# Kernel tuning notes

Hardware: AMD Instinct MI355X
Metric: run time of the kernel (lower is better)

## Reference

```python
import jax, jax.numpy as jnp
import numpy as np

NUM_LAYERS = 2
VOCAB = 32000
IN_FEAT = 256          # embedding dim is IN_FEAT-1, +1 for cue scalar
HIDDEN = 256
ATN = 64               # hardcoded atn_feature_size in GraphConvolution
CLASSES = 2
B, N = 8, 2048


def setup_inputs() -> dict:
    key = jax.random.key(0)
    ks = jax.random.split(key, 12)
    x = jax.random.randint(ks[0], (B, N), 0, VOCAB, dtype=jnp.int32)
    cue = jax.random.randint(ks[1], (B, N), 0, 2, dtype=jnp.int32)
    adj = (jax.random.uniform(ks[2], (B, N, N)) < 0.01).astype(jnp.float32)
    s = 1.0 / np.sqrt(HIDDEN)
    emb_table = jax.random.normal(ks[3], (VOCAB, IN_FEAT - 1), jnp.float32) * 0.02
    Wh = jax.random.uniform(ks[4], (IN_FEAT, HIDDEN), jnp.float32, -s, s)
    bh = jax.random.uniform(ks[5], (HIDDEN,), jnp.float32, -s, s)
    Wq = jax.random.uniform(ks[6], (HIDDEN, ATN), jnp.float32, -s, s)
    Wk = jax.random.uniform(ks[7], (HIDDEN, ATN), jnp.float32, -s, s)
    Wv = jax.random.uniform(ks[8], (HIDDEN, HIDDEN), jnp.float32, -s, s)
    gcb = jax.random.uniform(ks[9], (HIDDEN,), jnp.float32, -s, s)
    Wc = jax.random.uniform(ks[10], (HIDDEN, CLASSES), jnp.float32, -s, s)
    bc = jax.random.uniform(ks[11], (CLASSES,), jnp.float32, -s, s)
    return {"x": x, "cue": cue, "adj": adj, "emb_table": emb_table,
            "Wh": Wh, "bh": bh, "Wq": Wq, "Wk": Wk, "Wv": Wv,
            "gcb": gcb, "Wc": Wc, "bc": bc}


def graph_attention_layer(h, adj, Wq, Wk, Wv, gcb):
    # h: [B,N,H]; adj: [B,N,N] binary. Per node i: softmax over neighbors j of
    # (Wk h_j) . (Wq h_i), weighted sum of Wv h_j. Zero-degree nodes get 0 (pre-bias).
    q = jnp.einsum('bnh,ha->bna', h, Wq)        # [B,N,A]
    k = jnp.einsum('bnh,ha->bna', h, Wk)        # [B,N,A]
    v = jnp.einsum('bnh,hg->bng', h, Wv)        # [B,N,H]
    logits = jnp.einsum('bia,bja->bij', q, k)   # [B,N,N]
    mask = adj > 0
    attn = jax.nn.softmax(jnp.where(mask, logits, -1e9), axis=-1)
    out = jnp.einsum('bij,bjh->bih', attn, v)   # [B,N,H]
    has_nbr = jnp.any(mask, axis=-1, keepdims=True)  # [B,N,1]
    return jnp.where(has_nbr, out, 0.0) + gcb


def reference(x, cue, adj, emb_table, Wh, bh, Wq, Wk, Wv, gcb, Wc, bc):
    emb = emb_table[x]                                   # [B,N,IN_FEAT-1]
    feats = jnp.concatenate([emb, cue.astype(jnp.float32)[..., None]], axis=-1)
    h = jax.nn.relu(jnp.einsum('bnf,fh->bnh', feats, Wh) + bh)
    for _ in range(NUM_LAYERS):
        h = jax.nn.sigmoid(graph_attention_layer(h, adj, Wq, Wk, Wv, gcb))
    logits = jnp.einsum('bnh,hc->bnc', h, Wc) + bc
    return jax.nn.softmax(logits, axis=-1)
```

## Files before the change

### kernel.cpp

```cpp
#include <hip/hip_runtime.h>
#include <hip/hip_bf16.h>


#define NB 8
#define NN 2048
#define ROWS (NB * NN)
#define MAXD 64

typedef float f4 __attribute__((ext_vector_type(4)));
typedef short bf8 __attribute__((ext_vector_type(8)));
typedef unsigned short u16;
typedef u16 us4 __attribute__((ext_vector_type(4)));
typedef u16 us8 __attribute__((ext_vector_type(8)));

__device__ __forceinline__ float sigmoidf_(float x) { return 1.f / (1.f + __expf(-x)); }
__device__ __forceinline__ u16 f2bf(float f) {
    unsigned u = __float_as_uint(f);
    u += 0x7fffu + ((u >> 16) & 1u);
    return (u16)(u >> 16);
}
__device__ __forceinline__ float bf2f(u16 h) {
    return __uint_as_float(((unsigned)h) << 16);
}

#define PACK_BLKS 96
#define EMB_BLKS 512

__global__ __launch_bounds__(256) void k_fused_front(
        const int* __restrict__ x, const int* __restrict__ cue,
        const float* __restrict__ adj, const float* __restrict__ emb,
        const float* __restrict__ Wh, const float* __restrict__ bh,
        const float* __restrict__ Wq, const float* __restrict__ Wk,
        const float* __restrict__ Wv,
        u16* __restrict__ hB, u16* __restrict__ Wpt,
        int* __restrict__ deg, int* __restrict__ nbr) {
    __shared__ float As[32 * 64];
    __shared__ float Ws[32 * 128];
    int bid = blockIdx.x;
    int t = threadIdx.x;

    if (bid < PACK_BLKS) {
        int idxp = bid * 256 + t;
#pragma unroll
        for (int r = 0; r < 4; ++r) {
            int i = idxp + r * PACK_BLKS * 256;
            int c = i >> 8, f = i & 255;
            float v;
            if (c < 64)       v = Wq[f * 64 + c];
            else if (c < 128) v = Wk[f * 64 + (c - 64)];
            else              v = Wv[f * 256 + (c - 128)];
            Wpt[i] = f2bf(v);
        }
        return;
    }

    if (bid < PACK_BLKS + EMB_BLKS) {
        int eb = bid - PACK_BLKS;
        int rt = eb >> 1, ct = eb & 1;
        int row0 = rt * 64, col0 = ct * 128;
        int sm = t & 63, skg = t >> 6;
        int swc = (t & 31) * 4, swk = t >> 5;
        int tx = t & 15, ty = t >> 4;
        int xr = x[row0 + sm];
        float cv = (float)cue[row0 + sm];
        const float* er = emb + (size_t)xr * 255;

        float acc[4][8];
#pragma unroll
        for (int i = 0; i < 4; ++i)
#pragma unroll
            for (int j = 0; j < 8; ++j) acc[i][j] = 0.f;

        for (int kc = 0; kc < 256; kc += 32) {
            int kb = skg * 8;
#pragma unroll
            for (int u = 0; u < 8; ++u) {
                int f = kc + kb + u;
                As[(kb + u) * 64 + sm] = (f < 255) ? er[f] : cv;
            }
#pragma unroll
            for (int r = 0; r < 4; ++r) {
                int kk = swk + r * 8;
                f4 w = *(const f4*)(Wh + (size_t)(kc + kk) * 256 + col0 + swc);
                *(f4*)&Ws[kk * 128 + swc] = w;
            }
            __syncthreads();
#pragma unroll
            for (int k = 0; k < 32; ++k) {
                f4 av = *(f4*)&As[k * 64 + ty * 4];
                f4 w0 = *(f4*)&Ws[k * 128 + tx * 8];
                f4 w1 = *(f4*)&Ws[k * 128 + tx * 8 + 4];
                float a[4] = {av.x, av.y, av.z, av.w};
                float w[8] = {w0.x, w0.y, w0.z, w0.w, w1.x, w1.y, w1.z, w1.w};
#pragma unroll
                for (int i = 0; i < 4; ++i)
#pragma unroll
                    for (int j = 0; j < 8; ++j) acc[i][j] += a[i] * w[j];
            }
            __syncthreads();
        }
        f4 b0 = *(const f4*)(bh + col0 + tx * 8);
        f4 b1 = *(const f4*)(bh + col0 + tx * 8 + 4);
        float bb[8] = {b0.x, b0.y, b0.z, b0.w, b1.x, b1.y, b1.z, b1.w};
#pragma unroll
        for (int i = 0; i < 4; ++i) {
            int row = row0 + ty * 4 + i;
            us8 o;
#pragma unroll
            for (int j = 0; j < 8; ++j) o[j] = f2bf(fmaxf(acc[i][j] + bb[j], 0.f));
            *(us8*)(hB + (size_t)row * 256 + col0 + tx * 8) = o;
        }
        return;
    }

    int row = bid - (PACK_BLKS + EMB_BLKS);
    const f4* ar4 = (const f4*)(adj + (size_t)row * NN);
    int* cnt = (int*)As;
    if (t == 0) *cnt = 0;
    __syncthreads();
    int* nr = nbr + (size_t)row * MAXD;
#pragma unroll
    for (int it = 0; it < 2; ++it) {
        int idx = it * 256 + t;
        f4 vv = __builtin_nontemporal_load(ar4 + idx);
        if (vv.x > 0.f) { int p = atomicAdd(cnt, 1); if (p < MAXD) nr[p] = idx * 4 + 0; }
        if (vv.y > 0.f) { int p = atomicAdd(cnt, 1); if (p < MAXD) nr[p] = idx * 4 + 1; }
        if (vv.z > 0.f) { int p = atomicAdd(cnt, 1); if (p < MAXD) nr[p] = idx * 4 + 2; }
        if (vv.w > 0.f) { int p = atomicAdd(cnt, 1); if (p < MAXD) nr[p] = idx * 4 + 3; }
    }
    __syncthreads();
    if (t == 0) deg[row] = (*cnt < MAXD) ? *cnt : MAXD;
}

__global__ __launch_bounds__(256) void k_qkv_mfma(const u16* __restrict__ hB,
                                                  const u16* __restrict__ Wpt,
                                                  float* __restrict__ q,
                                                  u16* __restrict__ kv) {
    __shared__ u16 As[64 * 40];
    __shared__ u16 Bs[128 * 40];
    int t = threadIdx.x;
    int col0 = blockIdx.x * 128, row0 = blockIdx.y * 64;
    int wave = t >> 6, lane = t & 63;
    int l16 = lane & 15, quad = lane >> 4;

    f4 acc[4][2];
#pragma unroll
    for (int i = 0; i < 4; ++i) { acc[i][0] = (f4){0,0,0,0}; acc[i][1] = (f4){0,0,0,0}; }

    int ar = t >> 2, ao = (t & 3) * 8;
    int bc = t >> 1, bo = (t & 1) * 16;

    for (int kc = 0; kc < 256; kc += 32) {
        us8 av  = *(const us8*)(hB  + (size_t)(row0 + ar) * 256 + kc + ao);
        us8 bv0 = *(const us8*)(Wpt + (size_t)(col0 + bc) * 256 + kc + bo);
        us8 bv1 = *(const us8*)(Wpt + (size_t)(col0 + bc) * 256 + kc + bo + 8);
        __syncthreads();
        *(us8*)&As[ar * 40 + ao] = av;
        *(us8*)&Bs[bc * 40 + bo] = bv0;
        *(us8*)&Bs[bc * 40 + bo + 8] = bv1;
        __syncthreads();
        bf8 afr[4], bfr[2];
#pragma unroll
        for (int mt = 0; mt < 4; ++mt)
            afr[mt] = *(bf8*)&As[(mt * 16 + l16) * 40 + quad * 8];
#pragma unroll
        for (int nt = 0; nt < 2; ++nt)
            bfr[nt] = *(bf8*)&Bs[((wave * 2 + nt) * 16 + l16) * 40 + quad * 8];
#pragma unroll
        for (int mt = 0; mt < 4; ++mt)
#pragma unroll
            for (int nt = 0; nt < 2; ++nt)
                acc[mt][nt] = __builtin_amdgcn_mfma_f32_16x16x32_bf16(
                    afr[mt], bfr[nt], acc[mt][nt], 0, 0, 0);
    }
#pragma unroll
    for (int mt = 0; mt < 4; ++mt)
#pragma unroll
        for (int nt = 0; nt < 2; ++nt) {
            int c = col0 + (wave * 2 + nt) * 16 + l16;
#pragma unroll
            for (int reg = 0; reg < 4; ++reg) {
                int r = row0 + mt * 16 + quad * 4 + reg;
                float val = acc[mt][nt][reg];
                if (c < 64) q[(size_t)r * 64 + c] = val;
                else        kv[(size_t)r * 320 + (c - 64)] = f2bf(val);
            }
        }
}

template <bool WRITE_OUT>
__global__ __launch_bounds__(256) void k_attn(const float* __restrict__ q,
                                              const u16* __restrict__ kv,
                                              const int* __restrict__ deg,
                                              const int* __restrict__ nbr,
                                              const float* __restrict__ gcb,
                                              const float* __restrict__ Wc,
                                              const float* __restrict__ bc,
                                              u16* __restrict__ hB,
                                              float* __restrict__ out) {
    int wave = threadIdx.x >> 6;
    int lane = threadIdx.x & 63;
    int row = blockIdx.x * 4 + wave;
    int d = deg[row];
    int l16 = lane & 15;
    f4 g4 = *(const f4*)(gcb + lane * 4);
    float h0, h1, h2, h3;
    if (d == 0) {
        h0 = sigmoidf_(g4.x); h1 = sigmoidf_(g4.y);
        h2 = sigmoidf_(g4.z); h3 = sigmoidf_(g4.w);
    } else {
        f4 q4 = *(const f4*)(q + (size_t)row * 64 + l16 * 4);
        const int* jl = nbr + (size_t)row * MAXD;
        int bbase = row & ~(NN - 1);
        float m = -1e30f, s = 0.f;
        f4 a = {0, 0, 0, 0};
        for (int e = 0; e < d; e += 4) {
            int idx = e + (lane >> 4);
            int jg = jl[idx < d ? idx : 0];
            const u16* kr = kv + (size_t)(bbase + jg) * 320;
            us4 kq = *(const us4*)(kr + l16 * 4);
            float p = q4.x * bf2f(kq.x) + q4.y * bf2f(kq.y)
                    + q4.z * bf2f(kq.z) + q4.w * bf2f(kq.w);
            p += __shfl_xor(p, 1); p += __shfl_xor(p, 2);
            p += __shfl_xor(p, 4); p += __shfl_xor(p, 8);
            if (idx >= d) p = -1e30f;
            float p0 = __shfl(p, 0),  p1 = __shfl(p, 16);
            float p2 = __shfl(p, 32), p3 = __shfl(p, 48);
            int j0 = __shfl(jg, 0),  j1 = __shfl(jg, 16);
            int j2 = __shfl(jg, 32), j3 = __shfl(jg, 48);
            float mx = fmaxf(fmaxf(p0, p1), fmaxf(p2, p3));
            float mn = fmaxf(m, mx);
            float scale = __expf(m - mn);
            float w0 = __expf(p0 - mn), w1 = __expf(p1 - mn);
            float w2 = __expf(p2 - mn), w3 = __expf(p3 - mn);
            s = s * scale + ((w0 + w1) + (w2 + w3));
            us4 u0 = *(const us4*)(kv + (size_t)(bbase + j0) * 320 + 64 + lane * 4);
            us4 u1 = *(const us4*)(kv + (size_t)(bbase + j1) * 320 + 64 + lane * 4);
            us4 u2 = *(const us4*)(kv + (size_t)(bbase + j2) * 320 + 64 + lane * 4);
            us4 u3 = *(const us4*)(kv + (size_t)(bbase + j3) * 320 + 64 + lane * 4);
            a.x = a.x * scale + w0 * bf2f(u0.x) + w1 * bf2f(u1.x) + w2 * bf2f(u2.x) + w3 * bf2f(u3.x);
            a.y = a.y * scale + w0 * bf2f(u0.y) + w1 * bf2f(u1.y) + w2 * bf2f(u2.y) + w3 * bf2f(u3.y);
            a.z = a.z * scale + w0 * bf2f(u0.z) + w1 * bf2f(u1.z) + w2 * bf2f(u2.z) + w3 * bf2f(u3.z);
            a.w = a.w * scale + w0 * bf2f(u0.w) + w1 * bf2f(u1.w) + w2 * bf2f(u2.w) + w3 * bf2f(u3.w);
            m = mn;
        }
        float inv = 1.f / s;
        h0 = sigmoidf_(a.x * inv + g4.x);
        h1 = sigmoidf_(a.y * inv + g4.y);
        h2 = sigmoidf_(a.z * inv + g4.z);
        h3 = sigmoidf_(a.w * inv + g4.w);
    }
    if (!WRITE_OUT) {
        us4 o;
        o.x = f2bf(h0); o.y = f2bf(h1); o.z = f2bf(h2); o.w = f2bf(h3);
        *(us4*)(hB + (size_t)row * 256 + lane * 4) = o;
    } else {
        f4 wc0 = *(const f4*)(Wc + lane * 8);
        f4 wc1 = *(const f4*)(Wc + lane * 8 + 4);
        float pa = h0 * wc0.x + h1 * wc0.z + h2 * wc1.x + h3 * wc1.z;
        float pb = h0 * wc0.y + h1 * wc0.w + h2 * wc1.y + h3 * wc1.w;
#pragma unroll
        for (int off = 32; off; off >>= 1) {
            pa += __shfl_xor(pa, off);
            pb += __shfl_xor(pb, off);
        }
        if (lane == 0) {
            float l0 = pa + bc[0], l1 = pb + bc[1];
            float mx = fmaxf(l0, l1);
            float e0 = __expf(l0 - mx), e1 = __expf(l1 - mx);
            float inv = 1.f / (e0 + e1);
            out[(size_t)row * 2 + 0] = e0 * inv;
            out[(size_t)row * 2 + 1] = e1 * inv;
        }
    }
}

extern "C" void kernel_launch(void* const* d_in, const int* in_sizes, int n_in,
                              void* d_out, int out_size, void* d_ws, size_t ws_size,
                              hipStream_t stream) {
    const int*   x    = (const int*)d_in[0];
    const int*   cue  = (const int*)d_in[1];
    const float* adj  = (const float*)d_in[2];
    const float* emb  = (const float*)d_in[3];
    const float* Wh   = (const float*)d_in[4];
    const float* bh   = (const float*)d_in[5];
    const float* Wq   = (const float*)d_in[6];
    const float* Wk   = (const float*)d_in[7];
    const float* Wv   = (const float*)d_in[8];
    const float* gcb  = (const float*)d_in[9];
    const float* Wc   = (const float*)d_in[10];
    const float* bc   = (const float*)d_in[11];
    float* out = (float*)d_out;

    char* w = (char*)d_ws;
    u16*   hB  = (u16*)w;                 w += (size_t)ROWS * 256 * 2;
    float* q   = (float*)w;               w += (size_t)ROWS * 64 * 4;
    u16*   kv  = (u16*)w;                 w += (size_t)ROWS * 320 * 2;
    u16*   Wpt = (u16*)w;                 w += (size_t)384 * 256 * 2;
    int*   deg = (int*)w;                 w += (size_t)ROWS * 4;
    int*   nbr = (int*)w;

    k_fused_front<<<PACK_BLKS + EMB_BLKS + ROWS, 256, 0, stream>>>(
        x, cue, adj, emb, Wh, bh, Wq, Wk, Wv, hB, Wpt, deg, nbr);
    k_qkv_mfma<<<dim3(3, ROWS / 64), 256, 0, stream>>>(hB, Wpt, q, kv);
    k_attn<false><<<ROWS / 4, 256, 0, stream>>>(q, kv, deg, nbr, gcb, Wc, bc, hB, out);
    k_qkv_mfma<<<dim3(3, ROWS / 64), 256, 0, stream>>>(hB, Wpt, q, kv);
    k_attn<true><<<ROWS / 4, 256, 0, stream>>>(q, kv, deg, nbr, gcb, Wc, bc, hB, out);
}
```

Baseline: 326.9 us.

## Switch intermediates to fp16 with dot2 attention, LDS-free QKV MFMA, batch-interleaved rows

Replaces bf16 intermediates with fp16 throughout. Q is also stored in fp16 inside a single packed qkv buffer, replacing the separate fp32 q array. The QKV GEMM drops its shared-memory staging and barriers and loads MFMA fragments directly from global memory. The attention kernel uses packed fdot2 with byte-perm shuffles for the score and value accumulation, and remaps block indices so consecutive blocks cover different batches. Together these aim to cut memory traffic and ALU work, at the cost of fp16 range and precision and uncoalesced direct fragment loads.

Measured after the change: 340.0 us. 4.0% more time.

```diff
diff --git a/kernel.cpp b/kernel.cpp
--- a/kernel.cpp
+++ b/kernel.cpp
@@ -8,20 +8,25 @@
 #define MAXD 64
 
 typedef float f4 __attribute__((ext_vector_type(4)));
-typedef short bf8 __attribute__((ext_vector_type(8)));
+typedef _Float16 hf;
+typedef _Float16 h2 __attribute__((ext_vector_type(2)));
+typedef _Float16 h4 __attribute__((ext_vector_type(4)));
+typedef _Float16 h8 __attribute__((ext_vector_type(8)));
+typedef unsigned int  u32;
 typedef unsigned short u16;
-typedef u16 us4 __attribute__((ext_vector_type(4)));
-typedef u16 us8 __attribute__((ext_vector_type(8)));
 
 __device__ __forceinline__ float sigmoidf_(float x) { return 1.f / (1.f + __expf(-x)); }
-__device__ __forceinline__ u16 f2bf(float f) {
-    unsigned u = __float_as_uint(f);
-    u += 0x7fffu + ((u >> 16) & 1u);
-    return (u16)(u >> 16);
-}
-__device__ __forceinline__ float bf2f(u16 h) {
-    return __uint_as_float(((unsigned)h) << 16);
-}
+__device__ __forceinline__ h2 u2h(u32 u) { union { u32 u; h2 h; } c; c.u = u; return c.h; }
+
+__device__ __forceinline__ float dot2_(h2 a, h2 b, float c) {
+#if __has_builtin(__builtin_amdgcn_fdot2)
+    return __builtin_amdgcn_fdot2(a, b, c, false);
+#else
+    return c + (float)a.x * (float)b.x + (float)a.y * (float)b.y;
+#endif
+}
+__device__ __forceinline__ u32 permlo_(u32 hi, u32 lo) { return __builtin_amdgcn_perm(hi, lo, 0x05040100u); }
+__device__ __forceinline__ u32 permhi_(u32 hi, u32 lo) { return __builtin_amdgcn_perm(hi, lo, 0x07060302u); }
 
 #define PACK_BLKS 96
 #define EMB_BLKS 512
@@ -32,7 +37,7 @@
         const float* __restrict__ Wh, const float* __restrict__ bh,
         const float* __restrict__ Wq, const float* __restrict__ Wk,
         const float* __restrict__ Wv,
-        u16* __restrict__ hB, u16* __restrict__ Wpt,
+        hf* __restrict__ hB, hf* __restrict__ Wpt,
         int* __restrict__ deg, int* __restrict__ nbr) {
     __shared__ float As[32 * 64];
     __shared__ float Ws[32 * 128];
@@ -49,7 +54,7 @@
             if (c < 64)       v = Wq[f * 64 + c];
             else if (c < 128) v = Wk[f * 64 + (c - 64)];
             else              v = Wv[f * 256 + (c - 128)];
-            Wpt[i] = f2bf(v);
+            Wpt[i] = (hf)v;
         }
         return;
     }
@@ -105,10 +110,10 @@
 #pragma unroll
         for (int i = 0; i < 4; ++i) {
             int row = row0 + ty * 4 + i;
-            us8 o;
-#pragma unroll
-            for (int j = 0; j < 8; ++j) o[j] = f2bf(fmaxf(acc[i][j] + bb[j], 0.f));
-            *(us8*)(hB + (size_t)row * 256 + col0 + tx * 8) = o;
+            h8 o;
+#pragma unroll
+            for (int j = 0; j < 8; ++j) o[j] = (hf)fmaxf(acc[i][j] + bb[j], 0.f);
+            *(h8*)(hB + (size_t)row * 256 + col0 + tx * 8) = o;
         }
         return;
     }
@@ -132,12 +137,9 @@
     if (t == 0) deg[row] = (*cnt < MAXD) ? *cnt : MAXD;
 }
 
-__global__ __launch_bounds__(256) void k_qkv_mfma(const u16* __restrict__ hB,
-                                                  const u16* __restrict__ Wpt,
-                                                  float* __restrict__ q,
-                                                  u16* __restrict__ kv) {
-    __shared__ u16 As[64 * 40];
-    __shared__ u16 Bs[128 * 40];
+__global__ __launch_bounds__(256) void k_qkv_mfma(const hf* __restrict__ hB,
+                                                  const hf* __restrict__ Wpt,
+                                                  hf* __restrict__ qkvB) {
     int t = threadIdx.x;
     int col0 = blockIdx.x * 128, row0 = blockIdx.y * 64;
     int wave = t >> 6, lane = t & 63;
@@ -147,30 +149,23 @@
 #pragma unroll
     for (int i = 0; i < 4; ++i) { acc[i][0] = (f4){0,0,0,0}; acc[i][1] = (f4){0,0,0,0}; }
 
-    int ar = t >> 2, ao = (t & 3) * 8;
-    int bc = t >> 1, bo = (t & 1) * 16;
-
+    const hf* a0 = hB + (size_t)(row0 + l16) * 256 + quad * 8;
+    const hf* b0 = Wpt + (size_t)(col0 + wave * 32 + l16) * 256 + quad * 8;
+
+#pragma unroll
     for (int kc = 0; kc < 256; kc += 32) {
-        us8 av  = *(const us8*)(hB  + (size_t)(row0 + ar) * 256 + kc + ao);
-        us8 bv0 = *(const us8*)(Wpt + (size_t)(col0 + bc) * 256 + kc + bo);
-        us8 bv1 = *(const us8*)(Wpt + (size_t)(col0 + bc) * 256 + kc + bo + 8);
-        __syncthreads();
-        *(us8*)&As[ar * 40 + ao] = av;
-        *(us8*)&Bs[bc * 40 + bo] = bv0;
-        *(us8*)&Bs[bc * 40 + bo + 8] = bv1;
-        __syncthreads();
-        bf8 afr[4], bfr[2];
+        h8 afr[4], bfr[2];
 #pragma unroll
         for (int mt = 0; mt < 4; ++mt)
-            afr[mt] = *(bf8*)&As[(mt * 16 + l16) * 40 + quad * 8];
+            afr[mt] = *(const h8*)(a0 + (size_t)(mt * 16) * 256 + kc);
 #pragma unroll
         for (int nt = 0; nt < 2; ++nt)
-            bfr[nt] = *(bf8*)&Bs[((wave * 2 + nt) * 16 + l16) * 40 + quad * 8];
+            bfr[nt] = *(const h8*)(b0 + (size_t)(nt * 16) * 256 + kc);
 #pragma unroll
         for (int mt = 0; mt < 4; ++mt)
 #pragma unroll
             for (int nt = 0; nt < 2; ++nt)
-                acc[mt][nt] = __builtin_amdgcn_mfma_f32_16x16x32_bf16(
+                acc[mt][nt] = __builtin_amdgcn_mfma_f32_16x16x32_f16(
                     afr[mt], bfr[nt], acc[mt][nt], 0, 0, 0);
     }
 #pragma unroll
@@ -181,46 +176,44 @@
 #pragma unroll
             for (int reg = 0; reg < 4; ++reg) {
                 int r = row0 + mt * 16 + quad * 4 + reg;
-                float val = acc[mt][nt][reg];
-                if (c < 64) q[(size_t)r * 64 + c] = val;
-                else        kv[(size_t)r * 320 + (c - 64)] = f2bf(val);
+                qkvB[(size_t)r * 384 + c] = (hf)acc[mt][nt][reg];
             }
         }
 }
 
 template <bool WRITE_OUT>
-__global__ __launch_bounds__(256) void k_attn(const float* __restrict__ q,
-                                              const u16* __restrict__ kv,
+__global__ __launch_bounds__(256) void k_attn(const hf* __restrict__ qkvB,
                                               const int* __restrict__ deg,
                                               const int* __restrict__ nbr,
                                               const float* __restrict__ gcb,
                                               const float* __restrict__ Wc,
                                               const float* __restrict__ bc,
-                                              u16* __restrict__ hB,
+                                              hf* __restrict__ hB,
                                               float* __restrict__ out) {
     int wave = threadIdx.x >> 6;
     int lane = threadIdx.x & 63;
-    int row = blockIdx.x * 4 + wave;
+    int bid = blockIdx.x;
+    int row = (bid & 7) * NN + (bid >> 3) * 4 + wave;
     int d = deg[row];
-    int l16 = lane & 15;
+    int l16 = lane & 15, quad = lane >> 4;
     f4 g4 = *(const f4*)(gcb + lane * 4);
-    float h0, h1, h2, h3;
+    float h0, h1, h2v, h3;
     if (d == 0) {
         h0 = sigmoidf_(g4.x); h1 = sigmoidf_(g4.y);
-        h2 = sigmoidf_(g4.z); h3 = sigmoidf_(g4.w);
+        h2v = sigmoidf_(g4.z); h3 = sigmoidf_(g4.w);
     } else {
-        f4 q4 = *(const f4*)(q + (size_t)row * 64 + l16 * 4);
+        uint2 qq = *(const uint2*)(qkvB + (size_t)row * 384 + l16 * 4);
+        h2 q01 = u2h(qq.x), q23 = u2h(qq.y);
         const int* jl = nbr + (size_t)row * MAXD;
         int bbase = row & ~(NN - 1);
         float m = -1e30f, s = 0.f;
         f4 a = {0, 0, 0, 0};
         for (int e = 0; e < d; e += 4) {
-            int idx = e + (lane >> 4);
+            int idx = e + quad;
             int jg = jl[idx < d ? idx : 0];
-            const u16* kr = kv + (size_t)(bbase + jg) * 320;
-            us4 kq = *(const us4*)(kr + l16 * 4);
-            float p = q4.x * bf2f(kq.x) + q4.y * bf2f(kq.y)
-                    + q4.z * bf2f(kq.z) + q4.w * bf2f(kq.w);
+            const hf* kr = qkvB + (size_t)(bbase + jg) * 384;
+            uint2 kq = *(const uint2*)(kr + 64 + l16 * 4);
+            float p = dot2_(u2h(kq.x), q01, dot2_(u2h(kq.y), q23, 0.f));
             p += __shfl_xor(p, 1); p += __shfl_xor(p, 2);
             p += __shfl_xor(p, 4); p += __shfl_xor(p, 8);
             if (idx >= d) p = -1e30f;
@@ -234,31 +227,36 @@
             float w0 = __expf(p0 - mn), w1 = __expf(p1 - mn);
             float w2 = __expf(p2 - mn), w3 = __expf(p3 - mn);
             s = s * scale + ((w0 + w1) + (w2 + w3));
-            us4 u0 = *(const us4*)(kv + (size_t)(bbase + j0) * 320 + 64 + lane * 4);
-            us4 u1 = *(const us4*)(kv + (size_t)(bbase + j1) * 320 + 64 + lane * 4);
-            us4 u2 = *(const us4*)(kv + (size_t)(bbase + j2) * 320 + 64 + lane * 4);
-            us4 u3 = *(const us4*)(kv + (size_t)(bbase + j3) * 320 + 64 + lane * 4);
-            a.x = a.x * scale + w0 * bf2f(u0.x) + w1 * bf2f(u1.x) + w2 * bf2f(u2.x) + w3 * bf2f(u3.x);
-            a.y = a.y * scale + w0 * bf2f(u0.y) + w1 * bf2f(u1.y) + w2 * bf2f(u2.y) + w3 * bf2f(u3.y);
-            a.z = a.z * scale + w0 * bf2f(u0.z) + w1 * bf2f(u1.z) + w2 * bf2f(u2.z) + w3 * bf2f(u3.z);
-            a.w = a.w * scale + w0 * bf2f(u0.w) + w1 * bf2f(u1.w) + w2 * bf2f(u2.w) + w3 * bf2f(u3.w);
+            h2 w01; w01.x = (hf)w0; w01.y = (hf)w1;
+            h2 w23; w23.x = (hf)w2; w23.y = (hf)w3;
+            uint2 u0 = *(const uint2*)(qkvB + (size_t)(bbase + j0) * 384 + 128 + lane * 4);
+            uint2 u1 = *(const uint2*)(qkvB + (size_t)(bbase + j1) * 384 + 128 + lane * 4);
+            uint2 u2v = *(const uint2*)(qkvB + (size_t)(bbase + j2) * 384 + 128 + lane * 4);
+            uint2 u3 = *(const uint2*)(qkvB + (size_t)(bbase + j3) * 384 + 128 + lane * 4);
+            a.x = dot2_(u2h(permlo_(u1.x, u0.x)), w01,
+                  dot2_(u2h(permlo_(u3.x, u2v.x)), w23, a.x * scale));
+            a.y = dot2_(u2h(permhi_(u1.x, u0.x)), w01,
+                  dot2_(u2h(permhi_(u3.x, u2v.x)), w23, a.y * scale));
+            a.z = dot2_(u2h(permlo_(u1.y, u0.y)), w01,
+                  dot2_(u2h(permlo_(u3.y, u2v.y)), w23, a.z * scale));
+            a.w = dot2_(u2h(permhi_(u1.y, u0.y)), w01,
+                  dot2_(u2h(permhi_(u3.y, u2v.y)), w23, a.w * scale));
             m = mn;
         }
         float inv = 1.f / s;
         h0 = sigmoidf_(a.x * inv + g4.x);
         h1 = sigmoidf_(a.y * inv + g4.y);
-        h2 = sigmoidf_(a.z * inv + g4.z);
+        h2v = sigmoidf_(a.z * inv + g4.z);
         h3 = sigmoidf_(a.w * inv + g4.w);
     }
     if (!WRITE_OUT) {
-        us4 o;
-        o.x = f2bf(h0); o.y = f2bf(h1); o.z = f2bf(h2); o.w = f2bf(h3);
-        *(us4*)(hB + (size_t)row * 256 + lane * 4) = o;
+        h4 o; o.x = (hf)h0; o.y = (hf)h1; o.z = (hf)h2v; o.w = (hf)h3;
+        *(h4*)(hB + (size_t)row * 256 + lane * 4) = o;
     } else {
         f4 wc0 = *(const f4*)(Wc + lane * 8);
         f4 wc1 = *(const f4*)(Wc + lane * 8 + 4);
-        float pa = h0 * wc0.x + h1 * wc0.z + h2 * wc1.x + h3 * wc1.z;
-        float pb = h0 * wc0.y + h1 * wc0.w + h2 * wc1.y + h3 * wc1.w;
+        float pa = h0 * wc0.x + h1 * wc0.z + h2v * wc1.x + h3 * wc1.z;
+        float pb = h0 * wc0.y + h1 * wc0.w + h2v * wc1.y + h3 * wc1.w;
 #pragma unroll
         for (int off = 32; off; off >>= 1) {
             pa += __shfl_xor(pa, off);
@@ -293,17 +291,16 @@
     float* out = (float*)d_out;
 
     char* w = (char*)d_ws;
-    u16*   hB  = (u16*)w;                 w += (size_t)ROWS * 256 * 2;
-    float* q   = (float*)w;               w += (size_t)ROWS * 64 * 4;
-    u16*   kv  = (u16*)w;                 w += (size_t)ROWS * 320 * 2;
-    u16*   Wpt = (u16*)w;                 w += (size_t)384 * 256 * 2;
-    int*   deg = (int*)w;                 w += (size_t)ROWS * 4;
-    int*   nbr = (int*)w;
+    hf*  hB   = (hf*)w;   w += (size_t)ROWS * 256 * 2;
+    hf*  qkvB = (hf*)w;   w += (size_t)ROWS * 384 * 2;
+    hf*  Wpt  = (hf*)w;   w += (size_t)384 * 256 * 2;
+    int* deg  = (int*)w;  w += (size_t)ROWS * 4;
+    int* nbr  = (int*)w;
 
     k_fused_front<<<PACK_BLKS + EMB_BLKS + ROWS, 256, 0, stream>>>(
         x, cue, adj, emb, Wh, bh, Wq, Wk, Wv, hB, Wpt, deg, nbr);
-    k_qkv_mfma<<<dim3(3, ROWS / 64), 256, 0, stream>>>(hB, Wpt, q, kv);
-    k_attn<false><<<ROWS / 4, 256, 0, stream>>>(q, kv, deg, nbr, gcb, Wc, bc, hB, out);
-    k_qkv_mfma<<<dim3(3, ROWS / 64), 256, 0, stream>>>(hB, Wpt, q, kv);
-    k_attn<true><<<ROWS / 4, 256, 0, stream>>>(q, kv, deg, nbr, gcb, Wc, bc, hB, out);
-}
+    k_qkv_mfma<<<dim3(3, ROWS / 64), 256, 0, stream>>>(hB, Wpt, qkvB);
+    k_attn<false><<<ROWS / 4, 256, 0, stream>>>(qkvB, deg, nbr, gcb, Wc, bc, hB, out);
+    k_qkv_mfma<<<dim3(3, ROWS / 64), 256, 0, stream>>>(hB, Wpt, qkvB);
+    k_attn<true><<<ROWS / 4, 256, 0, stream>>>(qkvB, deg, nbr, gcb, Wc, bc, hB, out);
+}
```
